# Kernel tuning notes

Hardware: AMD Instinct MI355X
Metric: run time of the kernel (lower is better)

## Reference

```python
import jax, jax.numpy as jnp
import numpy as np

N_NODES = 25000
N_EDGES = 400000
FEAT = 128
HID = 64
HEADS = 4
NUM_CLASSES = 2
NUM_GRAPHS = 64


def setup_inputs() -> dict:
    key = jax.random.key(0)
    ks = jax.random.split(key, 16)
    x = jax.random.normal(ks[0], (N_NODES, FEAT), dtype=jnp.float32)
    edge_index = jax.random.randint(ks[1], (2, N_EDGES), 0, N_NODES, dtype=jnp.int32)
    batch = jnp.sort(jax.random.randint(ks[2], (N_NODES,), 0, NUM_GRAPHS, dtype=jnp.int32))
    s = 1.0 / np.sqrt(FEAT)
    sh = 1.0 / np.sqrt(HID)
    shc = 1.0 / np.sqrt(HID * HEADS)
    return {
        "x": x,
        "edge_index": edge_index,
        "batch": batch,
        # conv1: GraphConv(FEAT -> HID): lin_rel (bias) on aggregated neighbors + lin_root (no bias)
        "W1_rel": jax.random.uniform(ks[3], (FEAT, HID), jnp.float32, -s, s),
        "b1": jnp.zeros((HID,), jnp.float32),
        "W1_root": jax.random.uniform(ks[4], (FEAT, HID), jnp.float32, -s, s),
        # conv3: GATConv(HID -> HID, heads=HEADS), concat output [N, HEADS*HID]
        "Wg": jax.random.uniform(ks[5], (HID, HEADS * HID), jnp.float32, -sh, sh),
        "att_src": jax.random.uniform(ks[6], (HEADS, HID), jnp.float32, -sh, sh),
        "att_dst": jax.random.uniform(ks[7], (HEADS, HID), jnp.float32, -sh, sh),
        "bg": jnp.zeros((HEADS * HID,), jnp.float32),
        # conv5: GraphConv(HEADS*HID -> HID)
        "W5_rel": jax.random.uniform(ks[8], (HEADS * HID, HID), jnp.float32, -shc, shc),
        "b5": jnp.zeros((HID,), jnp.float32),
        "W5_root": jax.random.uniform(ks[9], (HEADS * HID, HID), jnp.float32, -shc, shc),
        # fc head
        "W_fc1": jax.random.uniform(ks[10], (HID, HID), jnp.float32, -sh, sh),
        "b_fc1": jnp.zeros((HID,), jnp.float32),
        "W_fc2": jax.random.uniform(ks[11], (HID, NUM_CLASSES), jnp.float32, -sh, sh),
        "b_fc2": jnp.zeros((NUM_CLASSES,), jnp.float32),
    }


def _graph_conv(h, src, dst, W_rel, b, W_root):
    # PyG GraphConv (aggr='add'): out_i = W_rel @ sum_{j->i} h_j + b + W_root @ h_i
    agg = jax.ops.segment_sum(h[src], dst, num_segments=N_NODES)
    return agg @ W_rel + b + h @ W_root


def _gat_conv(h, src, dst, Wg, att_src, att_dst, bg):
    # GATConv with default add_self_loops=True; eval mode (no attn dropout)
    n = h.shape[0]
    loop = jnp.arange(n, dtype=src.dtype)
    si = jnp.concatenate([src, loop])
    di = jnp.concatenate([dst, loop])
    xl = (h @ Wg).reshape(n, HEADS, HID)              # [N, H, C]
    a_s = jnp.sum(xl * att_src, axis=-1)              # [N, H]
    a_d = jnp.sum(xl * att_dst, axis=-1)              # [N, H]
    e = jax.nn.leaky_relu(a_s[si] + a_d[di], 0.2)     # [E', H]
    m = jax.ops.segment_max(e, di, num_segments=n)
    p = jnp.exp(e - m[di])
    denom = jax.ops.segment_sum(p, di, num_segments=n)
    alpha = p / denom[di]                             # segment softmax over incoming edges
    out = jax.ops.segment_sum(alpha[:, :, None] * xl[si], di, num_segments=n)
    return out.reshape(n, HEADS * HID) + bg


def reference(x, edge_index, batch, W1_rel, b1, W1_root, Wg, att_src, att_dst, bg,
              W5_rel, b5, W5_root, W_fc1, b_fc1, W_fc2, b_fc2):
    src, dst = edge_index[0], edge_index[1]
    h = jax.nn.relu(_graph_conv(x, src, dst, W1_rel, b1, W1_root))
    h = jax.nn.relu(_gat_conv(h, src, dst, Wg, att_src, att_dst, bg))
    h = jax.nn.relu(_graph_conv(h, src, dst, W5_rel, b5, W5_root))
    g = jax.ops.segment_sum(h, batch, num_segments=NUM_GRAPHS)   # global_add_pool
    g = jax.nn.relu(g @ W_fc1 + b_fc1)
    return jax.nn.sigmoid(g @ W_fc2 + b_fc2)
```

## Files before the change

### kernel.cpp

```cpp
#include <hip/hip_runtime.h>
#include <math.h>

#define N_NODES 25000
#define N_EDGES 400000
#define FEAT 128
#define HID 64
#define HEADS 4
#define HH 256
#define NUM_GRAPHS 64
#define BUCKET 96
#define HS 1601536
#define NPH 25600

typedef unsigned short ushort_t;
typedef unsigned int uint_t;
typedef __attribute__((ext_vector_type(8))) short short8;
typedef __attribute__((ext_vector_type(4))) float f32x4;

__device__ __forceinline__ float lrelu(float x){ return x > 0.f ? x : 0.2f*x; }

__device__ __forceinline__ ushort_t f2bf(float f){
  uint_t u = __float_as_uint(f);
  return (ushort_t)((u + 0x7fffu + ((u >> 16) & 1u)) >> 16);
}
#define BF_LO(u) __uint_as_float((u) << 16)
#define BF_HI(u) __uint_as_float((u) & 0xffff0000u)

__global__ __launch_bounds__(256) void k_fill(
    const int* __restrict__ src, const int* __restrict__ dst,
    int* __restrict__ cnt, int* __restrict__ slot,
    const float* __restrict__ W1_rel, const float* __restrict__ W1_root,
    const float* __restrict__ W5_rel, const float* __restrict__ W5_root,
    const float* __restrict__ Wg,
    ushort_t* __restrict__ wc1b, ushort_t* __restrict__ wc5b,
    ushort_t* __restrict__ wgb)
{
  const int e = blockIdx.x*256 + threadIdx.x;
  if (blockIdx.x < 64){
    {
      int j=e&7, lane=(e>>3)&63, kc=(e>>9)&3, nt=e>>11;
      int k = kc*32 + (lane>>4)*8 + j, n = nt*16 + (lane&15);
      float v = (n < 64) ? W1_rel[k*64 + n] : W1_root[k*64 + n - 64];
      wc1b[e] = f2bf(v);
    }
    {
      int j=e&7, lane=(e>>3)&63, kt=(e>>9)&1, nt=e>>10;
      int k = kt*32 + (lane>>4)*8 + j, n = nt*16 + (lane&15);
      wgb[e] = f2bf(Wg[k*HH + n]);
    }
    #pragma unroll
    for (int e5 = e; e5 < 32768; e5 += 16384){
      int j=e5&7, lane=(e5>>3)&63, kc=(e5>>9)&7, nt=e5>>12;
      int k = kc*32 + (lane>>4)*8 + j, n = nt*16 + (lane&15);
      float v = (n < 64) ? W5_rel[k*64 + n] : W5_root[k*64 + n - 64];
      wc5b[e5] = f2bf(v);
    }
  }
  if (e < N_EDGES){
    int d = dst[e];
    int pos = atomicAdd(&cnt[d], 1);
    if (pos < BUCKET) slot[(size_t)d*BUCKET + pos] = src[e];
  }
}

__global__ __launch_bounds__(256) void conv1_mfma(
    const float* __restrict__ X, const ushort_t* __restrict__ wc1b,
    const float* __restrict__ bias,
    ushort_t* __restrict__ out_rel_b, float* __restrict__ out_root)
{
  const int wid  = __builtin_amdgcn_readfirstlane(threadIdx.x >> 6);
  const int lane = threadIdx.x & 63;
  const int quad = lane >> 4, col = lane & 15;
  const int nb = blockIdx.x*64 + wid*16;
  if (nb >= N_NODES) return;
  const int row = min(nb + col, N_NODES-1);
  const float* __restrict__ xr = X + (size_t)row*FEAT + quad*8;
  short8 a[4];
  #pragma unroll
  for (int kc = 0; kc < 4; kc++){
    #pragma unroll
    for (int j = 0; j < 8; j++)
      ((ushort_t*)&a[kc])[j] = f2bf(xr[kc*32 + j]);
  }
  #pragma unroll
  for (int nt = 0; nt < 8; nt++){
    f32x4 d = {0.f,0.f,0.f,0.f};
    #pragma unroll
    for (int kc = 0; kc < 4; kc++){
      short8 b = *(const short8*)(wc1b + ((size_t)(nt*4+kc)*64 + lane)*8);
      d = __builtin_amdgcn_mfma_f32_16x16x32_bf16(a[kc], b, d, 0, 0, 0);
    }
    if (nt < 4){
      #pragma unroll
      for (int r = 0; r < 4; r++){
        const int node = nb + quad*4 + r;
        if (node < N_NODES)
          out_rel_b[(size_t)node*HID + nt*16 + col] = f2bf(d[r]);
      }
    } else {
      const float bv = bias[(nt-4)*16 + col];
      #pragma unroll
      for (int r = 0; r < 4; r++){
        const int node = nb + quad*4 + r;
        if (node < N_NODES)
          out_root[(size_t)node*HID + (nt-4)*16 + col] = d[r] + bv;
      }
    }
  }
}

__global__ __launch_bounds__(256) void conv5_mfma(
    const ushort_t* __restrict__ h2b_hm, const ushort_t* __restrict__ wc5b,
    const float* __restrict__ bias,
    ushort_t* __restrict__ out_rel_b, float* __restrict__ out_root)
{
  const int wid  = __builtin_amdgcn_readfirstlane(threadIdx.x >> 6);
  const int lane = threadIdx.x & 63;
  const int quad = lane >> 4, col = lane & 15;
  const int nb = blockIdx.x*64 + wid*16;
  if (nb >= N_NODES) return;
  const int row = nb + col;
  short8 a[8];
  #pragma unroll
  for (int kc = 0; kc < 8; kc++){
    const int k0 = kc*32 + quad*8;
    a[kc] = *(const short8*)(h2b_hm + (size_t)(k0>>6)*HS
                             + (size_t)row*HID + (k0&63));
  }
  #pragma unroll
  for (int nt = 0; nt < 8; nt++){
    f32x4 d = {0.f,0.f,0.f,0.f};
    #pragma unroll
    for (int kc = 0; kc < 8; kc++){
      short8 b = *(const short8*)(wc5b + ((size_t)(nt*8+kc)*64 + lane)*8);
      d = __builtin_amdgcn_mfma_f32_16x16x32_bf16(a[kc], b, d, 0, 0, 0);
    }
    if (nt < 4){
      #pragma unroll
      for (int r = 0; r < 4; r++){
        const int node = nb + quad*4 + r;
        if (node < N_NODES)
          out_rel_b[(size_t)node*HID + nt*16 + col] = f2bf(d[r]);
      }
    } else {
      const float bv = bias[(nt-4)*16 + col];
      #pragma unroll
      for (int r = 0; r < 4; r++){
        const int node = nb + quad*4 + r;
        if (node < N_NODES)
          out_root[(size_t)node*HID + (nt-4)*16 + col] = d[r] + bv;
      }
    }
  }
}

__global__ __launch_bounds__(256) void k3_mfma(
    const ushort_t* __restrict__ h1b, const ushort_t* __restrict__ wgb,
    const float* __restrict__ att_src, const float* __restrict__ att_dst,
    ushort_t* __restrict__ xlb_hm, float* __restrict__ a_s_hm,
    float* __restrict__ a_d_hm)
{
  const int wid  = __builtin_amdgcn_readfirstlane(threadIdx.x >> 6);
  const int lane = threadIdx.x & 63;
  const int quad = lane >> 4, col = lane & 15;
  const int nb = blockIdx.x*64 + wid*16;
  const ushort_t* arow = h1b + (size_t)(nb + col)*HID + quad*8;
  short8 a0 = *(const short8*)(arow);
  short8 a1 = *(const short8*)(arow + 32);
  float as_acc[4] = {0,0,0,0}, ad_acc[4] = {0,0,0,0};
  #pragma unroll
  for (int nt = 0; nt < 16; nt++){
    short8 b0 = *(const short8*)(wgb + ((size_t)(nt*2+0)*64 + lane)*8);
    short8 b1 = *(const short8*)(wgb + ((size_t)(nt*2+1)*64 + lane)*8);
    f32x4 d = {0.f, 0.f, 0.f, 0.f};
    d = __builtin_amdgcn_mfma_f32_16x16x32_bf16(a0, b0, d, 0, 0, 0);
    d = __builtin_amdgcn_mfma_f32_16x16x32_bf16(a1, b1, d, 0, 0, 0);
    const int h = nt >> 2;
    const float asv = att_src[h*HID + (nt & 3)*16 + col];
    const float adv = att_dst[h*HID + (nt & 3)*16 + col];
    #pragma unroll
    for (int r = 0; r < 4; r++){
      const int node = nb + quad*4 + r;
      if (node < N_NODES)
        xlb_hm[(size_t)h*HS + (size_t)node*HID + (nt&3)*16 + col] = f2bf(d[r]);
      as_acc[r] += d[r]*asv;
      ad_acc[r] += d[r]*adv;
    }
    if ((nt & 3) == 3){
      #pragma unroll
      for (int r = 0; r < 4; r++){
        float s1 = as_acc[r], s2 = ad_acc[r];
        #pragma unroll
        for (int off = 1; off < 16; off <<= 1){
          s1 += __shfl_xor(s1, off, 64);
          s2 += __shfl_xor(s2, off, 64);
        }
        const int node = nb + quad*4 + r;
        if (col == 0 && node < N_NODES){
          a_s_hm[h*NPH + node] = s1;
          a_d_hm[h*NPH + node] = s2;
        }
        as_acc[r] = 0.f; ad_acc[r] = 0.f;
      }
    }
  }
}

template<bool BF16OUT>
__global__ __launch_bounds__(256) void k_aggb(
    const int* __restrict__ cnt, const int* __restrict__ slot,
    const ushort_t* __restrict__ featb, const float* __restrict__ root,
    float* __restrict__ outf, ushort_t* __restrict__ outb)
{
  const int node = blockIdx.x*4 + (threadIdx.x >> 6);
  const int lane = threadIdx.x & 63;
  const int* __restrict__ sl = slot + (size_t)node*BUCKET;
  const int deg = min(cnt[node], BUCKET);
  float acc = root[(size_t)node*HID + lane];
  int e = 0;
  for (; e + 4 <= deg; e += 4){
    int sA = sl[e],   sB = sl[e+1];
    int sC = sl[e+2], sD = sl[e+3];
    acc += BF_LO((uint_t)featb[(size_t)sA*HID + lane]);
    acc += BF_LO((uint_t)featb[(size_t)sB*HID + lane]);
    acc += BF_LO((uint_t)featb[(size_t)sC*HID + lane]);
    acc += BF_LO((uint_t)featb[(size_t)sD*HID + lane]);
  }
  for (; e < deg; e++)
    acc += BF_LO((uint_t)featb[(size_t)sl[e]*HID + lane]);
  const float v = fmaxf(acc, 0.f);
  if (BF16OUT) outb[(size_t)node*HID + lane] = f2bf(v);
  else         outf[(size_t)node*HID + lane] = v;
}

__global__ __launch_bounds__(256) void k_gat_node(
    const int* __restrict__ cnt, const int* __restrict__ slot,
    const ushort_t* __restrict__ xlb_hm, const float* __restrict__ a_s_hm,
    const float* __restrict__ a_d_hm, const float* __restrict__ bg,
    ushort_t* __restrict__ h2b_hm)
{
  const int head = blockIdx.x & 3;
  const int node = (blockIdx.x >> 2)*16 + (threadIdx.x >> 4);
  if (node >= N_NODES) return;
  const int lane = threadIdx.x & 63;
  const int cl = lane & 15;
  const int gb = lane & 48;
  const int* __restrict__ sl = slot + (size_t)node*BUCKET;
  const int deg = min(cnt[node], BUCKET);
  const ushort_t* __restrict__ xlh = xlb_hm + (size_t)head*HS;
  const float* __restrict__ ash = a_s_hm + head*NPH;
  const float adh = a_d_hm[head*NPH + node];
  float acc0=0, acc1=0, acc2=0, acc3=0;
  float dsum = 0.f;
  for (int base = 0; base < deg; base += 16){
    float pme = 0.f; int sme = node;
    const int e = base + cl;
    if (e < deg){
      sme = sl[e];
      pme = __expf(lrelu(ash[sme] + adh));
    }
    dsum += pme;
    const int nsub = min(16, deg - base);
    int s = 0;
    for (; s + 2 <= nsub; s += 2){
      const float pA = __shfl(pme, gb + s, 64);
      const int   sA = __shfl(sme, gb + s, 64);
      const float pB = __shfl(pme, gb + s + 1, 64);
      const int   sB = __shfl(sme, gb + s + 1, 64);
      uint2 rA = ((const uint2*)(xlh + (size_t)sA*HID))[cl];
      uint2 rB = ((const uint2*)(xlh + (size_t)sB*HID))[cl];
      acc0 += pA*BF_LO(rA.x); acc1 += pA*BF_HI(rA.x);
      acc2 += pA*BF_LO(rA.y); acc3 += pA*BF_HI(rA.y);
      acc0 += pB*BF_LO(rB.x); acc1 += pB*BF_HI(rB.x);
      acc2 += pB*BF_LO(rB.y); acc3 += pB*BF_HI(rB.y);
    }
    if (s < nsub){
      const float pA = __shfl(pme, gb + s, 64);
      const int   sA = __shfl(sme, gb + s, 64);
      uint2 rA = ((const uint2*)(xlh + (size_t)sA*HID))[cl];
      acc0 += pA*BF_LO(rA.x); acc1 += pA*BF_HI(rA.x);
      acc2 += pA*BF_LO(rA.y); acc3 += pA*BF_HI(rA.y);
    }
  }
  #pragma unroll
  for (int off = 1; off < 16; off <<= 1) dsum += __shfl_xor(dsum, off, 64);
  const float pself = __expf(lrelu(ash[node] + adh));
  const float inv = 1.f / (dsum + pself);
  uint2 r = ((const uint2*)(xlh + (size_t)node*HID))[cl];
  acc0 += pself*BF_LO(r.x); acc1 += pself*BF_HI(r.x);
  acc2 += pself*BF_LO(r.y); acc3 += pself*BF_HI(r.y);
  const int col0 = head*HID + cl*4;
  const float ox = fmaxf(acc0*inv + bg[col0+0], 0.f);
  const float oy = fmaxf(acc1*inv + bg[col0+1], 0.f);
  const float oz = fmaxf(acc2*inv + bg[col0+2], 0.f);
  const float ow = fmaxf(acc3*inv + bg[col0+3], 0.f);
  uint2 o;
  o.x = (uint_t)f2bf(ox) | ((uint_t)f2bf(oy) << 16);
  o.y = (uint_t)f2bf(oz) | ((uint_t)f2bf(ow) << 16);
  ((uint2*)(h2b_hm + (size_t)head*HS + (size_t)node*HID))[cl] = o;
}

__global__ __launch_bounds__(256) void k_pool(
    const float* __restrict__ h3, const int* __restrict__ batch,
    float* __restrict__ g)
{
  const int w = blockIdx.x*4 + (threadIdx.x >> 6);
  const int j = threadIdx.x & 63;
  int n0 = w*64;
  if (n0 >= N_NODES) return;
  int n1 = min(n0+64, N_NODES);
  float acc = 0.f;
  int cur = batch[n0];
  for (int n = n0; n < n1; n++){
    int b = batch[n];
    if (b != cur){ atomicAdd(&g[cur*HID + j], acc); acc = 0.f; cur = b; }
    acc += h3[n*HID + j];
  }
  atomicAdd(&g[cur*HID + j], acc);
}

__global__ __launch_bounds__(256) void k_head(
    const float* __restrict__ g, const float* __restrict__ W1,
    const float* __restrict__ b1, const float* __restrict__ W2,
    const float* __restrict__ b2, float* __restrict__ out)
{
  __shared__ float gs[NUM_GRAPHS*HID];
  __shared__ float hh[NUM_GRAPHS*HID];
  for (int i = threadIdx.x; i < NUM_GRAPHS*HID; i += 256) gs[i] = g[i];
  __syncthreads();
  for (int t = threadIdx.x; t < NUM_GRAPHS*HID; t += 256){
    int b = t >> 6, j = t & 63;
    float acc = b1[j];
    for (int k = 0; k < HID; k++) acc += gs[b*HID+k]*W1[k*HID+j];
    hh[t] = fmaxf(acc, 0.f);
  }
  __syncthreads();
  for (int t = threadIdx.x; t < NUM_GRAPHS*2; t += 256){
    int b = t >> 1, c = t & 1;
    float acc = b2[c];
    for (int k = 0; k < HID; k++) acc += hh[b*HID+k]*W2[k*2+c];
    out[t] = 1.f / (1.f + __expf(-acc));
  }
}

extern "C" void kernel_launch(void* const* d_in, const int* in_sizes, int n_in,
                              void* d_out, int out_size, void* d_ws, size_t ws_size,
                              hipStream_t stream)
{
  const float* x       = (const float*)d_in[0];
  const int*   ei      = (const int*)d_in[1];
  const int*   batch   = (const int*)d_in[2];
  const float* W1_rel  = (const float*)d_in[3];
  const float* b1      = (const float*)d_in[4];
  const float* W1_root = (const float*)d_in[5];
  const float* Wg      = (const float*)d_in[6];
  const float* att_src = (const float*)d_in[7];
  const float* att_dst = (const float*)d_in[8];
  const float* bg      = (const float*)d_in[9];
  const float* W5_rel  = (const float*)d_in[10];
  const float* b5      = (const float*)d_in[11];
  const float* W5_root = (const float*)d_in[12];
  const float* W_fc1   = (const float*)d_in[13];
  const float* b_fc1   = (const float*)d_in[14];
  const float* W_fc2   = (const float*)d_in[15];
  const float* b_fc2   = (const float*)d_in[16];
  const int* src = ei;
  const int* dst = ei + N_EDGES;

  float* ws    = (float*)d_ws;
  ushort_t* xr_b   = (ushort_t*)ws;
  float*    hB     = ws +  800800;
  ushort_t* h1b    = (ushort_t*)(ws + 2402400);
  ushort_t* xlb_hm = (ushort_t*)(ws + 3203200);
  float*    a_s_hm = ws + 6406304;
  float*    a_d_hm = ws + 6508704;
  ushort_t* h2b_hm = (ushort_t*)(ws + 6611104);
  float*    g      = ws + 9814200;
  int*      cnt    = (int*)(ws + 9818296);
  ushort_t* wc1b   = (ushort_t*)(ws + 9843296);
  ushort_t* wc5b   = (ushort_t*)(ws + 9851488);
  ushort_t* wgb    = (ushort_t*)(ws + 9867872);
  int*      slot   = (int*)(ws + 9876064);
  float*    out    = (float*)d_out;

  hipMemsetAsync(g, 0, (4096 + N_NODES)*sizeof(float), stream);
  k_fill<<<(N_EDGES+255)/256,256,0,stream>>>(src, dst, cnt, slot,
      W1_rel, W1_root, W5_rel, W5_root, Wg, wc1b, wc5b, wgb);

  conv1_mfma<<<(N_NODES+63)/64,256,0,stream>>>(x, wc1b, b1, xr_b, hB);
  k_aggb<true><<<N_NODES/4,256,0,stream>>>(cnt, slot, xr_b, hB, nullptr, h1b);

  k3_mfma<<<(N_NODES+63)/64,256,0,stream>>>(h1b, wgb, att_src, att_dst,
                                            xlb_hm, a_s_hm, a_d_hm);
  k_gat_node<<<((N_NODES+15)/16)*HEADS,256,0,stream>>>(cnt, slot,
      xlb_hm, a_s_hm, a_d_hm, bg, h2b_hm);

  conv5_mfma<<<(N_NODES+63)/64,256,0,stream>>>(h2b_hm, wc5b, b5, xr_b, hB);
  k_aggb<false><<<N_NODES/4,256,0,stream>>>(cnt, slot, xr_b, hB, hB, nullptr);

  k_pool<<<(N_NODES/256)+1,256,0,stream>>>(hB, batch, g);
  k_head<<<1,256,0,stream>>>(g, W_fc1, b_fc1, W_fc2, b_fc2, out);
}
```

Baseline: 249.0 us.

## Fuse edge bucketing into conv1, zero buffers in init kernel, fold pooling into aggregation

Replaces the memset and the combined weight-convert/edge-fill kernel with a small init kernel that converts weights and zeroes the pool and count buffers. Edge bucketing now runs as extra blocks inside the conv1 MFMA launch, so the two independent jobs overlap. The final aggregation adds each node's result straight into the per-graph pool with atomics, which removes the k_pool kernel and the write of h3. The cost is many more contended atomics on the 64x64 pool buffer, since every node issues one per lane.

```diff
diff --git a/kernel.cpp b/kernel.cpp
--- a/kernel.cpp
+++ b/kernel.cpp
@@ -11,6 +11,7 @@
 #define BUCKET 96
 #define HS 1601536
 #define NPH 25600
+#define FILL_BLOCKS 1563
 
 typedef unsigned short ushort_t;
 typedef unsigned int uint_t;
@@ -26,52 +27,56 @@
 #define BF_LO(u) __uint_as_float((u) << 16)
 #define BF_HI(u) __uint_as_float((u) & 0xffff0000u)
 
-__global__ __launch_bounds__(256) void k_fill(
-    const int* __restrict__ src, const int* __restrict__ dst,
-    int* __restrict__ cnt, int* __restrict__ slot,
+__global__ __launch_bounds__(256) void k_init(
     const float* __restrict__ W1_rel, const float* __restrict__ W1_root,
     const float* __restrict__ W5_rel, const float* __restrict__ W5_root,
     const float* __restrict__ Wg,
     ushort_t* __restrict__ wc1b, ushort_t* __restrict__ wc5b,
-    ushort_t* __restrict__ wgb)
+    ushort_t* __restrict__ wgb, float* __restrict__ g )
 {
   const int e = blockIdx.x*256 + threadIdx.x;
-  if (blockIdx.x < 64){
-    {
-      int j=e&7, lane=(e>>3)&63, kc=(e>>9)&3, nt=e>>11;
-      int k = kc*32 + (lane>>4)*8 + j, n = nt*16 + (lane&15);
-      float v = (n < 64) ? W1_rel[k*64 + n] : W1_root[k*64 + n - 64];
-      wc1b[e] = f2bf(v);
-    }
-    {
-      int j=e&7, lane=(e>>3)&63, kt=(e>>9)&1, nt=e>>10;
-      int k = kt*32 + (lane>>4)*8 + j, n = nt*16 + (lane&15);
-      wgb[e] = f2bf(Wg[k*HH + n]);
-    }
-    #pragma unroll
-    for (int e5 = e; e5 < 32768; e5 += 16384){
-      int j=e5&7, lane=(e5>>3)&63, kc=(e5>>9)&7, nt=e5>>12;
-      int k = kc*32 + (lane>>4)*8 + j, n = nt*16 + (lane&15);
-      float v = (n < 64) ? W5_rel[k*64 + n] : W5_root[k*64 + n - 64];
-      wc5b[e5] = f2bf(v);
-    }
-  }
-  if (e < N_EDGES){
-    int d = dst[e];
-    int pos = atomicAdd(&cnt[d], 1);
-    if (pos < BUCKET) slot[(size_t)d*BUCKET + pos] = src[e];
-  }
-}
-
-__global__ __launch_bounds__(256) void conv1_mfma(
+  {
+    int j=e&7, lane=(e>>3)&63, kc=(e>>9)&3, nt=e>>11;
+    int k = kc*32 + (lane>>4)*8 + j, n = nt*16 + (lane&15);
+    float v = (n < 64) ? W1_rel[k*64 + n] : W1_root[k*64 + n - 64];
+    wc1b[e] = f2bf(v);
+  }
+  {
+    int j=e&7, lane=(e>>3)&63, kt=(e>>9)&1, nt=e>>10;
+    int k = kt*32 + (lane>>4)*8 + j, n = nt*16 + (lane&15);
+    wgb[e] = f2bf(Wg[k*HH + n]);
+  }
+  #pragma unroll
+  for (int e5 = e; e5 < 32768; e5 += 16384){
+    int j=e5&7, lane=(e5>>3)&63, kc=(e5>>9)&7, nt=e5>>12;
+    int k = kc*32 + (lane>>4)*8 + j, n = nt*16 + (lane&15);
+    float v = (n < 64) ? W5_rel[k*64 + n] : W5_root[k*64 + n - 64];
+    wc5b[e5] = f2bf(v);
+  }
+  int* z = (int*)g;
+  for (int i = e; i < 4096 + N_NODES; i += 16384) z[i] = 0;
+}
+
+__global__ __launch_bounds__(256) void k_c1_fill(
+    const int* __restrict__ src, const int* __restrict__ dst,
+    int* __restrict__ cnt, int* __restrict__ slot,
     const float* __restrict__ X, const ushort_t* __restrict__ wc1b,
     const float* __restrict__ bias,
     ushort_t* __restrict__ out_rel_b, float* __restrict__ out_root)
 {
+  if (blockIdx.x < FILL_BLOCKS){
+    const int e = blockIdx.x*256 + threadIdx.x;
+    if (e < N_EDGES){
+      int d = dst[e];
+      int pos = atomicAdd(&cnt[d], 1);
+      if (pos < BUCKET) slot[(size_t)d*BUCKET + pos] = src[e];
+    }
+    return;
+  }
   const int wid  = __builtin_amdgcn_readfirstlane(threadIdx.x >> 6);
   const int lane = threadIdx.x & 63;
   const int quad = lane >> 4, col = lane & 15;
-  const int nb = blockIdx.x*64 + wid*16;
+  const int nb = (blockIdx.x - FILL_BLOCKS)*64 + wid*16;
   if (nb >= N_NODES) return;
   const int row = min(nb + col, N_NODES-1);
   const float* __restrict__ xr = X + (size_t)row*FEAT + quad*8;
@@ -206,11 +211,12 @@
   }
 }
 
-template<bool BF16OUT>
+template<int MODE>
 __global__ __launch_bounds__(256) void k_aggb(
     const int* __restrict__ cnt, const int* __restrict__ slot,
     const ushort_t* __restrict__ featb, const float* __restrict__ root,
-    float* __restrict__ outf, ushort_t* __restrict__ outb)
+    const int* __restrict__ batch, float* __restrict__ g,
+    ushort_t* __restrict__ outb)
 {
   const int node = blockIdx.x*4 + (threadIdx.x >> 6);
   const int lane = threadIdx.x & 63;
@@ -229,8 +235,12 @@
   for (; e < deg; e++)
     acc += BF_LO((uint_t)featb[(size_t)sl[e]*HID + lane]);
   const float v = fmaxf(acc, 0.f);
-  if (BF16OUT) outb[(size_t)node*HID + lane] = f2bf(v);
-  else         outf[(size_t)node*HID + lane] = v;
+  if (MODE == 0){
+    outb[(size_t)node*HID + lane] = f2bf(v);
+  } else {
+    const int b = batch[node];
+    atomicAdd(&g[b*HID + lane], v);
+  }
 }
 
 __global__ __launch_bounds__(256) void k_gat_node(
@@ -298,25 +308,6 @@
   o.x = (uint_t)f2bf(ox) | ((uint_t)f2bf(oy) << 16);
   o.y = (uint_t)f2bf(oz) | ((uint_t)f2bf(ow) << 16);
   ((uint2*)(h2b_hm + (size_t)head*HS + (size_t)node*HID))[cl] = o;
-}
-
-__global__ __launch_bounds__(256) void k_pool(
-    const float* __restrict__ h3, const int* __restrict__ batch,
-    float* __restrict__ g)
-{
-  const int w = blockIdx.x*4 + (threadIdx.x >> 6);
-  const int j = threadIdx.x & 63;
-  int n0 = w*64;
-  if (n0 >= N_NODES) return;
-  int n1 = min(n0+64, N_NODES);
-  float acc = 0.f;
-  int cur = batch[n0];
-  for (int n = n0; n < n1; n++){
-    int b = batch[n];
-    if (b != cur){ atomicAdd(&g[cur*HID + j], acc); acc = 0.f; cur = b; }
-    acc += h3[n*HID + j];
-  }
-  atomicAdd(&g[cur*HID + j], acc);
 }
 
 __global__ __launch_bounds__(256) void k_head(
@@ -382,22 +373,26 @@
   ushort_t* wgb    = (ushort_t*)(ws + 9867872);
   int*      slot   = (int*)(ws + 9876064);
   float*    out    = (float*)d_out;
-
-  hipMemsetAsync(g, 0, (4096 + N_NODES)*sizeof(float), stream);
-  k_fill<<<(N_EDGES+255)/256,256,0,stream>>>(src, dst, cnt, slot,
-      W1_rel, W1_root, W5_rel, W5_root, Wg, wc1b, wc5b, wgb);
-
-  conv1_mfma<<<(N_NODES+63)/64,256,0,stream>>>(x, wc1b, b1, xr_b, hB);
-  k_aggb<true><<<N_NODES/4,256,0,stream>>>(cnt, slot, xr_b, hB, nullptr, h1b);
+  (void)cnt;
+
+  k_init<<<64,256,0,stream>>>(W1_rel, W1_root, W5_rel, W5_root, Wg,
+                              wc1b, wc5b, wgb, g);
+
+  k_c1_fill<<<FILL_BLOCKS + (N_NODES+63)/64,256,0,stream>>>(
+      src, dst, (int*)(ws + 9818296), (int*)(ws + 9876064),
+      x, wc1b, b1, xr_b, hB);
+
+  k_aggb<0><<<N_NODES/4,256,0,stream>>>((int*)(ws + 9818296), (int*)(ws + 9876064),
+      xr_b, hB, nullptr, nullptr, h1b);
 
   k3_mfma<<<(N_NODES+63)/64,256,0,stream>>>(h1b, wgb, att_src, att_dst,
                                             xlb_hm, a_s_hm, a_d_hm);
-  k_gat_node<<<((N_NODES+15)/16)*HEADS,256,0,stream>>>(cnt, slot,
-      xlb_hm, a_s_hm, a_d_hm, bg, h2b_hm);
+  k_gat_node<<<((N_NODES+15)/16)*HEADS,256,0,stream>>>((int*)(ws + 9818296),
+      (int*)(ws + 9876064), xlb_hm, a_s_hm, a_d_hm, bg, h2b_hm);
 
   conv5_mfma<<<(N_NODES+63)/64,256,0,stream>>>(h2b_hm, wc5b, b5, xr_b, hB);
-  k_aggb<false><<<N_NODES/4,256,0,stream>>>(cnt, slot, xr_b, hB, hB, nullptr);
-
-  k_pool<<<(N_NODES/256)+1,256,0,stream>>>(hB, batch, g);
+  k_aggb<1><<<N_NODES/4,256,0,stream>>>((int*)(ws + 9818296), (int*)(ws + 9876064),
+      xr_b, hB, batch, g, nullptr);
+
   k_head<<<1,256,0,stream>>>(g, W_fc1, b_fc1, W_fc2, b_fc2, out);
 }
```

Measured after the change: 253.5 us. Within noise of the previous version (+1.8%).
